# Kernel tuning notes

Hardware: AMD Instinct MI355X
Metric: run time of the kernel (lower is better)

The kernel has to match this reference:

```python
import jax, jax.numpy as jnp
import numpy as np

NUM_HEADS = 16


def _make_rope(n, half_dim, dtype=jnp.float32):
    # standard rotary frequencies: theta = 10000^{-2i/d}
    inv_freq = 1.0 / (10000.0 ** (np.arange(0, half_dim, dtype=np.float32) / half_dim))
    t = np.arange(n, dtype=np.float32)
    ang = np.outer(t, inv_freq)  # [n, half_dim]
    return jnp.asarray(np.cos(ang), dtype), jnp.asarray(np.sin(ang), dtype)


def setup_inputs() -> dict:
    key = jax.random.key(0)
    ks = jax.random.split(key, 10)
    B, N, C = 2, 2048, 1024
    H = NUM_HEADS
    hd = C // H
    q = jax.random.normal(ks[0], (B, N, C), jnp.float32)
    k = jax.random.normal(ks[1], (B, N, C), jnp.float32)
    v = jax.random.normal(ks[2], (B, N, C), jnp.float32)
    cos, sin = _make_rope(N, hd // 2)
    s = 1.0 / np.sqrt(C)
    Wq = jax.random.normal(ks[3], (C, C), jnp.float32) * s
    bq = jax.random.normal(ks[4], (C,), jnp.float32) * 0.02
    Wk = jax.random.normal(ks[5], (C, C), jnp.float32) * s
    bk = jax.random.normal(ks[6], (C,), jnp.float32) * 0.02
    Wv = jax.random.normal(ks[7], (C, C), jnp.float32) * s
    bv = jax.random.normal(ks[8], (C,), jnp.float32) * 0.02
    return {"q": q, "k": k, "v": v,
            "q_cos": cos, "q_sin": sin, "k_cos": cos, "k_sin": sin,
            "Wq": Wq, "bq": bq, "Wk": Wk, "bk": bk, "Wv": Wv, "bv": bv}


def _rope(x, cos, sin):
    # x: [B, H, N, hd]; pairs (x[...,2j], x[...,2j+1]) form complex numbers,
    # rotated by freqs_cis of shape [N, hd//2] (broadcast over B, H).
    xr = x[..., 0::2]
    xi = x[..., 1::2]
    c = cos[None, None]  # [1,1,N,hd//2]
    s = sin[None, None]
    out_r = xr * c - xi * s
    out_i = xr * s + xi * c
    return jnp.stack([out_r, out_i], axis=-1).reshape(x.shape)


def reference(q, k, v, q_cos, q_sin, k_cos, k_sin, Wq, bq, Wk, bk, Wv, bv):
    B, Nq, C = q.shape
    Nk = k.shape[1]
    H = NUM_HEADS
    hd = C // H
    scale = hd ** -0.5
    # QKV projections (torch nn.Linear: x @ W.T + b), split into heads
    qh = (q @ Wq.T + bq).reshape(B, Nq, H, hd).transpose(0, 2, 1, 3)  # [B,H,Nq,hd]
    kh = (k @ Wk.T + bk).reshape(B, Nk, H, hd).transpose(0, 2, 1, 3)
    vh = (v @ Wv.T + bv).reshape(B, Nk, H, hd).transpose(0, 2, 1, 3)
    # inline RoPE on q and k
    qh = _rope(qh, q_cos, q_sin)
    kh = _rope(kh, k_cos, k_sin)
    # scaled dot-product attention (mask=None, dropout=0, non-causal)
    scores = jnp.einsum('bhqd,bhkd->bhqk', qh, kh) * scale
    attn = jax.nn.softmax(scores, axis=-1)
    out = jnp.einsum('bhqk,bhkd->bhqd', attn, vh)
    # merge heads; NOTE: self.proj is never applied in the original forward
    return out.transpose(0, 2, 1, 3).reshape(B, Nq, C)
```

## Files before the change

### kernel.cpp

```cpp
#include <hip/hip_runtime.h>
#include <hip/hip_bf16.h>

typedef float f32x4 __attribute__((ext_vector_type(4)));
typedef short bf16x8 __attribute__((ext_vector_type(8)));

#define NSEQ 2048
#define CDIM 1024
#define NHEAD 16
#define HDIM 64
#define MROWS 4096
#define QSCALE 0.18033688011f
#define DEFER_THR 11.5416f

__device__ __forceinline__ unsigned short f2bf(float f) {
    unsigned int u = __builtin_bit_cast(unsigned int, f);
    u += 0x7FFFu + ((u >> 16) & 1u);
    return (unsigned short)(u >> 16);
}

__device__ __forceinline__ void gload16(const void* g, void* l) {
    __builtin_amdgcn_global_load_lds(
        (const __attribute__((address_space(1))) unsigned int*)g,
        (__attribute__((address_space(3))) unsigned int*)l, 16, 0, 0);
}

__global__ __launch_bounds__(256) void cvt6_kernel(
    const float* __restrict__ q, const float* __restrict__ k, const float* __restrict__ v,
    const float* __restrict__ wq, const float* __restrict__ wk, const float* __restrict__ wv,
    unsigned short* __restrict__ dq, unsigned short* __restrict__ dk, unsigned short* __restrict__ dv,
    unsigned short* __restrict__ dwq, unsigned short* __restrict__ dwk, unsigned short* __restrict__ dwv)
{
    int b = blockIdx.x;
    const float* s; unsigned short* d; int base;
    if (b < 4096)       { s = q;  d = dq;  base = b; }
    else if (b < 8192)  { s = k;  d = dk;  base = b - 4096; }
    else if (b < 12288) { s = v;  d = dv;  base = b - 8192; }
    else if (b < 13312) { s = wq; d = dwq; base = b - 12288; }
    else if (b < 14336) { s = wk; d = dwk; base = b - 13312; }
    else                { s = wv; d = dwv; base = b - 14336; }
    int i = (base * 256 + threadIdx.x) * 4;
    float4 t4 = *reinterpret_cast<const float4*>(s + i);
    ushort4 o;
    o.x = f2bf(t4.x); o.y = f2bf(t4.y); o.z = f2bf(t4.z); o.w = f2bf(t4.w);
    *reinterpret_cast<ushort4*>(d + i) = o;
}

__global__ __launch_bounds__(256) void gemm_rope_kernel(
    const unsigned short* __restrict__ Xq, const unsigned short* __restrict__ Xk,
    const unsigned short* __restrict__ Xv,
    const unsigned short* __restrict__ Wqb, const unsigned short* __restrict__ Wkb,
    const unsigned short* __restrict__ Wvb,
    const float* __restrict__ bq, const float* __restrict__ bk, const float* __restrict__ bv,
    const float* __restrict__ qcos, const float* __restrict__ qsin,
    const float* __restrict__ kcos, const float* __restrict__ ksin,
    unsigned short* __restrict__ Qh, unsigned short* __restrict__ Kh,
    unsigned short* __restrict__ VT)
{
    __shared__ unsigned short Al[128][72];
    __shared__ unsigned short Bl[128][72];

    const int tid  = threadIdx.x;
    const int wave = tid >> 6;
    const int lane = tid & 63;
    const int lr   = lane & 15;
    const int lg   = lane >> 4;
    const int lk   = lg * 8;
    const int wm   = wave >> 1;
    const int wn   = wave & 1;
    const int m0   = blockIdx.y * 128;
    const int j0   = blockIdx.x * 128;
    const int z    = blockIdx.z;

    const unsigned short* X = (z == 0) ? Xq : (z == 1) ? Xk : Xv;
    const unsigned short* W = (z == 0) ? Wqb : (z == 1) ? Wkb : Wvb;
    const float* bias = (z == 0) ? bq : (z == 1) ? bk : bv;
    const float* cosb = (z == 0) ? qcos : kcos;
    const float* sinb = (z == 0) ? qsin : ksin;

    f32x4 acc[4][4];
    const f32x4 zero4 = {0.f, 0.f, 0.f, 0.f};
    #pragma unroll
    for (int a = 0; a < 4; a++)
        #pragma unroll
        for (int b = 0; b < 4; b++) acc[a][b] = zero4;

    for (int k0 = 0; k0 < CDIM; k0 += 64) {
        __syncthreads();
        #pragma unroll
        for (int it = 0; it < 4; it++) {
            int c = tid + it * 256;
            int row = c >> 3, col = (c & 7) << 3;
            *reinterpret_cast<bf16x8*>(&Al[row][col]) =
                *reinterpret_cast<const bf16x8*>(X + (size_t)(m0 + row) * CDIM + k0 + col);
            *reinterpret_cast<bf16x8*>(&Bl[row][col]) =
                *reinterpret_cast<const bf16x8*>(W + (size_t)(j0 + row) * CDIM + k0 + col);
        }
        __syncthreads();
        #pragma unroll
        for (int ks = 0; ks < 2; ks++) {
            bf16x8 af[4], bfm[4];
            #pragma unroll
            for (int mi = 0; mi < 4; mi++)
                af[mi] = *reinterpret_cast<const bf16x8*>(&Al[wm * 64 + 16 * mi + lr][ks * 32 + lk]);
            #pragma unroll
            for (int ni = 0; ni < 4; ni++)
                bfm[ni] = *reinterpret_cast<const bf16x8*>(&Bl[wn * 64 + 16 * ni + lr][ks * 32 + lk]);
            #pragma unroll
            for (int mi = 0; mi < 4; mi++)
                #pragma unroll
                for (int ni = 0; ni < 4; ni++)
                    acc[mi][ni] = __builtin_amdgcn_mfma_f32_16x16x32_bf16(
                        af[mi], bfm[ni], acc[mi][ni], 0, 0, 0);
        }
    }

    #pragma unroll
    for (int mi = 0; mi < 4; mi++) {
        const int mbase = m0 + wm * 64 + 16 * mi + 4 * lg;
        #pragma unroll
        for (int ni = 0; ni < 4; ni++) {
            const int j  = j0 + wn * 64 + 16 * ni + lr;
            const float bj = bias[j];
            if (z == 2) {
                const int b = mbase >> 11, n = mbase & 2047;
                const int h = j >> 6, d = j & 63;
                ushort4 pk;
                pk.x = f2bf(acc[mi][ni][0] + bj);
                pk.y = f2bf(acc[mi][ni][1] + bj);
                pk.z = f2bf(acc[mi][ni][2] + bj);
                pk.w = f2bf(acc[mi][ni][3] + bj);
                *reinterpret_cast<ushort4*>(VT + ((size_t)((b * NHEAD + h) * HDIM + d) << 11) + n) = pk;
            } else {
                unsigned short* Out = (z == 0) ? Qh : Kh;
                const float scl = (z == 0) ? QSCALE : 1.0f;
                const int hi = (j & 63) >> 1;
                const float sg = (j & 1) ? 1.f : -1.f;
                float vv[4], pp[4];
                #pragma unroll
                for (int r = 0; r < 4; r++) vv[r] = acc[mi][ni][r] + bj;
                #pragma unroll
                for (int r = 0; r < 4; r++) pp[r] = __shfl_xor(vv[r], 1);
                #pragma unroll
                for (int r = 0; r < 4; r++) {
                    const int m = mbase + r;
                    const int b = m >> 11, n = m & 2047;
                    const float c = cosb[n * 32 + hi];
                    const float s = sinb[n * 32 + hi];
                    const float ov = fmaf(vv[r], c, pp[r] * (sg * s)) * scl;
                    Out[((size_t)((b * NHEAD + (j >> 6)) * NSEQ + n) << 6) + (j & 63)] = f2bf(ov);
                }
            }
        }
    }
}

__global__ __launch_bounds__(256) void attn_kernel(
    const unsigned short* __restrict__ Qh, const unsigned short* __restrict__ Kh,
    const unsigned short* __restrict__ VT, float* __restrict__ out)
{
    __shared__ unsigned char Ksm[2][8192];
    __shared__ unsigned char Vsm[2][8192];
    __shared__ unsigned char Psm[4][2304];

    const int tid  = threadIdx.x;
    const int wave = tid >> 6;
    const int lane = tid & 63;
    const int lr   = lane & 15;
    const int lg   = lane >> 4;
    const int bh   = blockIdx.y;
    const int q0w  = blockIdx.x * 64 + wave * 16;

    const unsigned short* Qb = Qh + (size_t)bh * NSEQ * HDIM;
    const char* Kb = (const char*)(Kh + (size_t)bh * NSEQ * HDIM);
    const char* Vb = (const char*)(VT + (size_t)bh * HDIM * NSEQ);

    bf16x8 qf[2];
    #pragma unroll
    for (int ks = 0; ks < 2; ks++)
        qf[ks] = *reinterpret_cast<const bf16x8*>(
            Qb + (size_t)(q0w + lr) * HDIM + ks * 32 + lg * 8);

    const f32x4 zero4 = {0.f, 0.f, 0.f, 0.f};
    f32x4 o[4];
    #pragma unroll
    for (int ni = 0; ni < 4; ni++) o[ni] = zero4;
    float mrun = -1e30f, lrun = 0.f;

    const int swz = (lr & 7) << 4;
    const int co0 = (lg * 16) ^ swz;
    const int co1 = (64 + lg * 16) ^ swz;

    const int sr7 = lane >> 3;
    const int scb = ((lane & 7) * 16) ^ (sr7 << 4);
    const int ch0 = wave * 2;

    auto stage = [&](int buf, int n0) {
        #pragma unroll
        for (int i = 0; i < 2; ++i) {
            const int row = (ch0 + i) * 8 + sr7;
            gload16(Kb + (size_t)(n0 + row) * 128 + scb, &Ksm[buf][(ch0 + i) * 1024]);
            gload16(Vb + (size_t)row * (NSEQ * 2) + (size_t)n0 * 2 + scb,
                    &Vsm[buf][(ch0 + i) * 1024]);
        }
    };

    stage(0, 0);
    __syncthreads();
    int cur = 0;

    for (int t = 0; t < 32; ++t) {
        if (t < 31) stage(cur ^ 1, (t + 1) * 64);

        f32x4 s[4];
        #pragma unroll
        for (int ni = 0; ni < 4; ni++) s[ni] = zero4;
        #pragma unroll
        for (int ks = 0; ks < 2; ks++) {
            const int co = ks ? co1 : co0;
            #pragma unroll
            for (int ni = 0; ni < 4; ni++) {
                bf16x8 kf = *reinterpret_cast<const bf16x8*>(
                    &Ksm[cur][(16 * ni + lr) * 128 + co]);
                s[ni] = __builtin_amdgcn_mfma_f32_16x16x32_bf16(kf, qf[ks], s[ni], 0, 0, 0);
            }
        }

        float tm = fmaxf(fmaxf(s[0][0], s[0][1]), fmaxf(s[0][2], s[0][3]));
        #pragma unroll
        for (int ni = 1; ni < 4; ni++)
            tm = fmaxf(tm, fmaxf(fmaxf(s[ni][0], s[ni][1]), fmaxf(s[ni][2], s[ni][3])));
        tm = fmaxf(tm, __shfl_xor(tm, 16));
        tm = fmaxf(tm, __shfl_xor(tm, 32));

        if (!__all(tm - mrun <= DEFER_THR)) {
            const float mnew  = fmaxf(mrun, tm);
            const float alpha = exp2f(mrun - mnew);
            mrun = mnew;
            lrun *= alpha;
            float afr[4];
            #pragma unroll
            for (int r = 0; r < 4; r++) afr[r] = __shfl(alpha, 4 * lg + r);
            #pragma unroll
            for (int ni = 0; ni < 4; ni++)
                #pragma unroll
                for (int r = 0; r < 4; r++) o[ni][r] *= afr[r];
        }

        float rs = 0.f;
        #pragma unroll
        for (int ni = 0; ni < 4; ni++)
            #pragma unroll
            for (int r = 0; r < 4; r++) {
                float p = exp2f(s[ni][r] - mrun);
                s[ni][r] = p;
                rs += p;
            }
        rs += __shfl_xor(rs, 16);
        rs += __shfl_xor(rs, 32);
        lrun += rs;

        unsigned char* pbase = &Psm[wave][lr * 144 + lg * 8];
        #pragma unroll
        for (int ni = 0; ni < 4; ni++) {
            ushort4 pk;
            pk.x = f2bf(s[ni][0]); pk.y = f2bf(s[ni][1]);
            pk.z = f2bf(s[ni][2]); pk.w = f2bf(s[ni][3]);
            *reinterpret_cast<ushort4*>(pbase + 32 * ni) = pk;
        }

        bf16x8 vf[2][4];
        #pragma unroll
        for (int ks = 0; ks < 2; ks++) {
            const int co = ks ? co1 : co0;
            #pragma unroll
            for (int ni = 0; ni < 4; ni++)
                vf[ks][ni] = *reinterpret_cast<const bf16x8*>(
                    &Vsm[cur][(16 * ni + lr) * 128 + co]);
        }
        asm volatile("s_waitcnt lgkmcnt(0)" ::: "memory");

        const unsigned char* prow = &Psm[wave][lr * 144];
        bf16x8 pa[2];
        pa[0] = *reinterpret_cast<const bf16x8*>(prow + lg * 16);
        pa[1] = *reinterpret_cast<const bf16x8*>(prow + 64 + lg * 16);

        #pragma unroll
        for (int ks = 0; ks < 2; ks++)
            #pragma unroll
            for (int ni = 0; ni < 4; ni++)
                o[ni] = __builtin_amdgcn_mfma_f32_16x16x32_bf16(
                    pa[ks], vf[ks][ni], o[ni], 0, 0, 0);

        __syncthreads();
        cur ^= 1;
    }

    float linv[4];
    #pragma unroll
    for (int r = 0; r < 4; r++) {
        float ll = __shfl(lrun, 4 * lg + r);
        linv[r] = 1.0f / ll;
    }
    const int b = bh >> 4, h = bh & 15;
    #pragma unroll
    for (int ni = 0; ni < 4; ni++)
        #pragma unroll
        for (int r = 0; r < 4; r++) {
            const int n = q0w + 4 * lg + r;
            out[((size_t)(b * NSEQ + n) << 10) + h * HDIM + 16 * ni + lr] =
                o[ni][r] * linv[r];
        }
}

extern "C" void kernel_launch(void* const* d_in, const int* in_sizes, int n_in,
                              void* d_out, int out_size, void* d_ws, size_t ws_size,
                              hipStream_t stream) {
    const float* q    = (const float*)d_in[0];
    const float* k    = (const float*)d_in[1];
    const float* v    = (const float*)d_in[2];
    const float* qcos = (const float*)d_in[3];
    const float* qsin = (const float*)d_in[4];
    const float* kcos = (const float*)d_in[5];
    const float* ksin = (const float*)d_in[6];
    const float* Wq   = (const float*)d_in[7];
    const float* bq   = (const float*)d_in[8];
    const float* Wk   = (const float*)d_in[9];
    const float* bk   = (const float*)d_in[10];
    const float* Wv   = (const float*)d_in[11];
    const float* bv   = (const float*)d_in[12];
    float* out = (float*)d_out;

    unsigned short* Xqb = (unsigned short*)d_ws;
    unsigned short* Xkb = Xqb + (size_t)MROWS * CDIM;
    unsigned short* Xvb = Xkb + (size_t)MROWS * CDIM;
    unsigned short* Wqb = Xvb + (size_t)MROWS * CDIM;
    unsigned short* Wkb = Wqb + (size_t)CDIM * CDIM;
    unsigned short* Wvb = Wkb + (size_t)CDIM * CDIM;
    unsigned short* Qhb = Wvb + (size_t)CDIM * CDIM;
    unsigned short* Khb = Qhb + (size_t)MROWS * CDIM;
    unsigned short* VTb = Khb + (size_t)MROWS * CDIM;

    cvt6_kernel<<<15360, 256, 0, stream>>>(q, k, v, Wq, Wk, Wv,
                                           Xqb, Xkb, Xvb, Wqb, Wkb, Wvb);

    dim3 gg(CDIM / 128, MROWS / 128, 3);
    gemm_rope_kernel<<<gg, 256, 0, stream>>>(Xqb, Xkb, Xvb, Wqb, Wkb, Wvb,
                                             bq, bk, bv, qcos, qsin, kcos, ksin,
                                             Qhb, Khb, VTb);

    attn_kernel<<<dim3(NSEQ / 64, 2 * NHEAD), 256, 0, stream>>>(Qhb, Khb, VTb, out);
}
```

Measured before the change: 166.8 us.

## Rewrite attention with 32x32x16 MFMA, register-resident P via permlane swap

The attention kernel moves from 16x16x32 MFMA tiles to 32x32x16 tiles, so each wave handles 32 query rows and each block covers 128 queries, halving the grid. The softmax probabilities are packed to bf16 with v_cvt_pk_bf16_f32 and rearranged into the A-operand layout with v_permlane32_swap. This removes the LDS round trip for P and its wait. It is meant to cut LDS traffic, per-tile sync and K/V reloads per query, at the cost of more accumulator registers and fewer blocks in flight.

```diff
diff --git a/kernel.cpp b/kernel.cpp
--- a/kernel.cpp
+++ b/kernel.cpp
@@ -2,6 +2,7 @@
 #include <hip/hip_bf16.h>
 
 typedef float f32x4 __attribute__((ext_vector_type(4)));
+typedef float f32x16 __attribute__((ext_vector_type(16)));
 typedef short bf16x8 __attribute__((ext_vector_type(8)));
 
 #define NSEQ 2048
@@ -16,6 +17,12 @@
     unsigned int u = __builtin_bit_cast(unsigned int, f);
     u += 0x7FFFu + ((u >> 16) & 1u);
     return (unsigned short)(u >> 16);
+}
+
+__device__ __forceinline__ unsigned pkbf(float lo, float hi_) {
+    unsigned r;
+    asm("v_cvt_pk_bf16_f32 %0, %1, %2" : "=v"(r) : "v"(lo), "v"(hi_));
+    return r;
 }
 
 __device__ __forceinline__ void gload16(const void* g, void* l) {
@@ -154,41 +161,35 @@
     }
 }
 
-__global__ __launch_bounds__(256) void attn_kernel(
+__global__ __launch_bounds__(256, 2) void attn_kernel(
     const unsigned short* __restrict__ Qh, const unsigned short* __restrict__ Kh,
     const unsigned short* __restrict__ VT, float* __restrict__ out)
 {
     __shared__ unsigned char Ksm[2][8192];
     __shared__ unsigned char Vsm[2][8192];
-    __shared__ unsigned char Psm[4][2304];
 
     const int tid  = threadIdx.x;
     const int wave = tid >> 6;
     const int lane = tid & 63;
-    const int lr   = lane & 15;
-    const int lg   = lane >> 4;
+    const int c    = lane & 31;
+    const int hi   = lane >> 5;
     const int bh   = blockIdx.y;
-    const int q0w  = blockIdx.x * 64 + wave * 16;
+    const int q0w  = blockIdx.x * 128 + wave * 32;
+    const int sw   = (c & 7) << 4;
 
     const unsigned short* Qb = Qh + (size_t)bh * NSEQ * HDIM;
     const char* Kb = (const char*)(Kh + (size_t)bh * NSEQ * HDIM);
     const char* Vb = (const char*)(VT + (size_t)bh * HDIM * NSEQ);
 
-    bf16x8 qf[2];
+    bf16x8 qf[4];
     #pragma unroll
-    for (int ks = 0; ks < 2; ks++)
-        qf[ks] = *reinterpret_cast<const bf16x8*>(
-            Qb + (size_t)(q0w + lr) * HDIM + ks * 32 + lg * 8);
-
-    const f32x4 zero4 = {0.f, 0.f, 0.f, 0.f};
-    f32x4 o[4];
-    #pragma unroll
-    for (int ni = 0; ni < 4; ni++) o[ni] = zero4;
+    for (int s = 0; s < 4; s++)
+        qf[s] = *reinterpret_cast<const bf16x8*>(
+            Qb + (size_t)(q0w + c) * HDIM + s * 16 + hi * 8);
+
+    const f32x16 z16 = {0,0,0,0,0,0,0,0,0,0,0,0,0,0,0,0};
+    f32x16 o0 = z16, o1 = z16;
     float mrun = -1e30f, lrun = 0.f;
-
-    const int swz = (lr & 7) << 4;
-    const int co0 = (lg * 16) ^ swz;
-    const int co1 = (64 + lg * 16) ^ swz;
 
     const int sr7 = lane >> 3;
     const int scb = ((lane & 7) * 16) ^ (sr7 << 4);
@@ -211,25 +212,23 @@
     for (int t = 0; t < 32; ++t) {
         if (t < 31) stage(cur ^ 1, (t + 1) * 64);
 
-        f32x4 s[4];
-        #pragma unroll
-        for (int ni = 0; ni < 4; ni++) s[ni] = zero4;
-        #pragma unroll
-        for (int ks = 0; ks < 2; ks++) {
-            const int co = ks ? co1 : co0;
-            #pragma unroll
-            for (int ni = 0; ni < 4; ni++) {
-                bf16x8 kf = *reinterpret_cast<const bf16x8*>(
-                    &Ksm[cur][(16 * ni + lr) * 128 + co]);
-                s[ni] = __builtin_amdgcn_mfma_f32_16x16x32_bf16(kf, qf[ks], s[ni], 0, 0, 0);
-            }
-        }
-
-        float tm = fmaxf(fmaxf(s[0][0], s[0][1]), fmaxf(s[0][2], s[0][3]));
-        #pragma unroll
-        for (int ni = 1; ni < 4; ni++)
-            tm = fmaxf(tm, fmaxf(fmaxf(s[ni][0], s[ni][1]), fmaxf(s[ni][2], s[ni][3])));
-        tm = fmaxf(tm, __shfl_xor(tm, 16));
+        f32x16 s0 = z16, s1 = z16;
+        #pragma unroll
+        for (int s = 0; s < 4; s++) {
+            const int cb = (32 * s + 16 * hi) ^ sw;
+            bf16x8 kf0 = *reinterpret_cast<const bf16x8*>(&Ksm[cur][c * 128 + cb]);
+            bf16x8 kf1 = *reinterpret_cast<const bf16x8*>(&Ksm[cur][(32 + c) * 128 + cb]);
+            s0 = __builtin_amdgcn_mfma_f32_32x32x16_bf16(kf0, qf[s], s0, 0, 0, 0);
+            s1 = __builtin_amdgcn_mfma_f32_32x32x16_bf16(kf1, qf[s], s1, 0, 0, 0);
+        }
+
+        float tmx[8];
+        #pragma unroll
+        for (int i = 0; i < 8; i++)
+            tmx[i] = fmaxf(fmaxf(s0[2 * i], s0[2 * i + 1]),
+                           fmaxf(s1[2 * i], s1[2 * i + 1]));
+        float tm = fmaxf(fmaxf(fmaxf(tmx[0], tmx[1]), fmaxf(tmx[2], tmx[3])),
+                         fmaxf(fmaxf(tmx[4], tmx[5]), fmaxf(tmx[6], tmx[7])));
         tm = fmaxf(tm, __shfl_xor(tm, 32));
 
         if (!__all(tm - mrun <= DEFER_THR)) {
@@ -237,79 +236,68 @@
             const float alpha = exp2f(mrun - mnew);
             mrun = mnew;
             lrun *= alpha;
-            float afr[4];
             #pragma unroll
-            for (int r = 0; r < 4; r++) afr[r] = __shfl(alpha, 4 * lg + r);
-            #pragma unroll
-            for (int ni = 0; ni < 4; ni++)
-                #pragma unroll
-                for (int r = 0; r < 4; r++) o[ni][r] *= afr[r];
-        }
-
-        float rs = 0.f;
-        #pragma unroll
-        for (int ni = 0; ni < 4; ni++)
-            #pragma unroll
-            for (int r = 0; r < 4; r++) {
-                float p = exp2f(s[ni][r] - mrun);
-                s[ni][r] = p;
-                rs += p;
+            for (int r = 0; r < 16; r++) {
+                const float ar = __shfl(alpha, (r & 3) + 8 * (r >> 2) + 4 * hi);
+                o0[r] *= ar;
+                o1[r] *= ar;
             }
-        rs += __shfl_xor(rs, 16);
+        }
+
+        #pragma unroll
+        for (int r = 0; r < 16; r++) s0[r] = exp2f(s0[r] - mrun);
+        #pragma unroll
+        for (int r = 0; r < 16; r++) s1[r] = exp2f(s1[r] - mrun);
+        float rsx[8];
+        #pragma unroll
+        for (int i = 0; i < 8; i++)
+            rsx[i] = (s0[2 * i] + s0[2 * i + 1]) + (s1[2 * i] + s1[2 * i + 1]);
+        float rs = ((rsx[0] + rsx[1]) + (rsx[2] + rsx[3])) +
+                   ((rsx[4] + rsx[5]) + (rsx[6] + rsx[7]));
         rs += __shfl_xor(rs, 32);
         lrun += rs;
 
-        unsigned char* pbase = &Psm[wave][lr * 144 + lg * 8];
-        #pragma unroll
-        for (int ni = 0; ni < 4; ni++) {
-            ushort4 pk;
-            pk.x = f2bf(s[ni][0]); pk.y = f2bf(s[ni][1]);
-            pk.z = f2bf(s[ni][2]); pk.w = f2bf(s[ni][3]);
-            *reinterpret_cast<ushort4*>(pbase + 32 * ni) = pk;
-        }
-
-        bf16x8 vf[2][4];
-        #pragma unroll
-        for (int ks = 0; ks < 2; ks++) {
-            const int co = ks ? co1 : co0;
-            #pragma unroll
-            for (int ni = 0; ni < 4; ni++)
-                vf[ks][ni] = *reinterpret_cast<const bf16x8*>(
-                    &Vsm[cur][(16 * ni + lr) * 128 + co]);
-        }
-        asm volatile("s_waitcnt lgkmcnt(0)" ::: "memory");
-
-        const unsigned char* prow = &Psm[wave][lr * 144];
-        bf16x8 pa[2];
-        pa[0] = *reinterpret_cast<const bf16x8*>(prow + lg * 16);
-        pa[1] = *reinterpret_cast<const bf16x8*>(prow + 64 + lg * 16);
-
-        #pragma unroll
-        for (int ks = 0; ks < 2; ks++)
-            #pragma unroll
-            for (int ni = 0; ni < 4; ni++)
-                o[ni] = __builtin_amdgcn_mfma_f32_16x16x32_bf16(
-                    pa[ks], vf[ks][ni], o[ni], 0, 0, 0);
+        unsigned pw[4][4];
+        #pragma unroll
+        for (int u = 0; u < 4; u++) {
+            const f32x16& sv = (u < 2) ? s0 : s1;
+            const int b = (u & 1) * 8;
+            unsigned x0 = pkbf(sv[b + 0], sv[b + 1]);
+            unsigned y0 = pkbf(sv[b + 4], sv[b + 5]);
+            asm("v_permlane32_swap_b32 %0, %1" : "+v"(x0), "+v"(y0));
+            unsigned x1 = pkbf(sv[b + 2], sv[b + 3]);
+            unsigned y1 = pkbf(sv[b + 6], sv[b + 7]);
+            asm("v_permlane32_swap_b32 %0, %1" : "+v"(x1), "+v"(y1));
+            pw[u][0] = x0; pw[u][1] = x1; pw[u][2] = y0; pw[u][3] = y1;
+        }
+
+        #pragma unroll
+        for (int u = 0; u < 4; u++) {
+            uint4 w;
+            w.x = pw[u][0]; w.y = pw[u][1]; w.z = pw[u][2]; w.w = pw[u][3];
+            bf16x8 pa = __builtin_bit_cast(bf16x8, w);
+            const int cb = (32 * u + 16 * hi) ^ sw;
+            bf16x8 vf0 = *reinterpret_cast<const bf16x8*>(&Vsm[cur][c * 128 + cb]);
+            bf16x8 vf1 = *reinterpret_cast<const bf16x8*>(&Vsm[cur][(32 + c) * 128 + cb]);
+            o0 = __builtin_amdgcn_mfma_f32_32x32x16_bf16(pa, vf0, o0, 0, 0, 0);
+            o1 = __builtin_amdgcn_mfma_f32_32x32x16_bf16(pa, vf1, o1, 0, 0, 0);
+        }
 
         __syncthreads();
         cur ^= 1;
     }
 
-    float linv[4];
-    #pragma unroll
-    for (int r = 0; r < 4; r++) {
-        float ll = __shfl(lrun, 4 * lg + r);
-        linv[r] = 1.0f / ll;
-    }
     const int b = bh >> 4, h = bh & 15;
     #pragma unroll
-    for (int ni = 0; ni < 4; ni++)
-        #pragma unroll
-        for (int r = 0; r < 4; r++) {
-            const int n = q0w + 4 * lg + r;
-            out[((size_t)(b * NSEQ + n) << 10) + h * HDIM + 16 * ni + lr] =
-                o[ni][r] * linv[r];
-        }
+    for (int r = 0; r < 16; r++) {
+        const int qrow = (r & 3) + 8 * (r >> 2) + 4 * hi;
+        const float li  = __shfl(lrun, qrow);
+        const float inv = 1.0f / li;
+        const int n = q0w + qrow;
+        float* op = out + ((size_t)(b * NSEQ + n) << 10) + h * HDIM + c;
+        op[0]  = o0[r] * inv;
+        op[32] = o1[r] * inv;
+    }
 }
 
 extern "C" void kernel_launch(void* const* d_in, const int* in_sizes, int n_in,
@@ -348,5 +336,5 @@
                                              bq, bk, bv, qcos, qsin, kcos, ksin,
                                              Qhb, Khb, VTb);
 
-    attn_kernel<<<dim3(NSEQ / 64, 2 * NHEAD), 256, 0, stream>>>(Qhb, Khb, VTb, out);
-}
+    attn_kernel<<<dim3(NSEQ / 128, 2 * NHEAD), 256, 0, stream>>>(Qhb, Khb, VTb, out);
+}
```

After: 137.6 us. -17.5%, faster.
